# Kernel tuning notes

Hardware: AMD Instinct MI355X
Metric: run time of the kernel (lower is better)

Reference implementation:

```python
import jax, jax.numpy as jnp
import numpy as np

IN_DIM = 5
HIDDEN = 256
NUM_LAYERS = 2
OUT_DIM = 3
B, T = 256, 512


def setup_inputs() -> dict:
    key = jax.random.key(0)
    ks = jax.random.split(key, 16)
    s = 1.0 / np.sqrt(HIDDEN)  # PyTorch LSTM init scale
    inp = {
        "x": jax.random.normal(ks[0], (B, T, IN_DIM), dtype=jnp.float32),
        # layer 0 (input dim 5)
        "Wih0": jax.random.uniform(ks[1], (4 * HIDDEN, IN_DIM), minval=-s, maxval=s),
        "Whh0": jax.random.uniform(ks[2], (4 * HIDDEN, HIDDEN), minval=-s, maxval=s),
        "bih0": jax.random.uniform(ks[3], (4 * HIDDEN,), minval=-s, maxval=s),
        "bhh0": jax.random.uniform(ks[4], (4 * HIDDEN,), minval=-s, maxval=s),
        # layer 1 (input dim HIDDEN)
        "Wih1": jax.random.uniform(ks[5], (4 * HIDDEN, HIDDEN), minval=-s, maxval=s),
        "Whh1": jax.random.uniform(ks[6], (4 * HIDDEN, HIDDEN), minval=-s, maxval=s),
        "bih1": jax.random.uniform(ks[7], (4 * HIDDEN,), minval=-s, maxval=s),
        "bhh1": jax.random.uniform(ks[8], (4 * HIDDEN,), minval=-s, maxval=s),
        # head: Linear(HIDDEN, 3)
        "Wh": jax.random.uniform(ks[9], (OUT_DIM, HIDDEN), minval=-s, maxval=s),
        "bh": jax.random.uniform(ks[10], (OUT_DIM,), minval=-s, maxval=s),
    }
    return inp


def _lstm_layer(x, Wih, Whh, bih, bhh):
    # x: [B, T, D_in] -> h_seq: [B, T, H]
    Bn, Tn, _ = x.shape
    H = Whh.shape[1]
    # precompute input contribution for all timesteps: [T, B, 4H]
    pre = jnp.einsum("btd,gd->tbg", x, Wih) + bih + bhh

    def step(carry, gates_in):
        h, c = carry
        gates = gates_in + h @ Whh.T  # [B, 4H]
        i, f, g, o = jnp.split(gates, 4, axis=-1)  # PyTorch gate order
        i = jax.nn.sigmoid(i)
        f = jax.nn.sigmoid(f)
        g = jnp.tanh(g)
        o = jax.nn.sigmoid(o)
        c = f * c + i * g
        h = o * jnp.tanh(c)
        return (h, c), h

    h0 = jnp.zeros((Bn, H), dtype=x.dtype)
    c0 = jnp.zeros((Bn, H), dtype=x.dtype)
    _, h_seq = jax.lax.scan(step, (h0, c0), pre)  # h_seq: [T, B, H]
    return jnp.transpose(h_seq, (1, 0, 2))  # [B, T, H]


def reference(x, Wih0, Whh0, bih0, bhh0, Wih1, Whh1, bih1, bhh1, Wh, bh):
    h = _lstm_layer(x, Wih0, Whh0, bih0, bhh0)
    h = _lstm_layer(h, Wih1, Whh1, bih1, bhh1)
    # head applied pointwise; only the last timestep is kept, so apply to last step
    last = h[:, -1, :]  # [B, H]
    y = jax.nn.sigmoid(jax.nn.relu(last) @ Wh.T + bh)  # [B, 3]
    return y[:, None, :]  # [B, 1, 3]
```

## Files before the change

### kernel.cpp

```cpp
#include <hip/hip_runtime.h>
#include <hip/hip_bf16.h>

typedef unsigned short u16;
typedef signed char i8;
typedef __attribute__((ext_vector_type(4))) float f32x4;
typedef __attribute__((ext_vector_type(4))) int i32x4;
typedef __attribute__((ext_vector_type(8))) short bf16x8;
typedef __attribute__((ext_vector_type(2))) unsigned int u32x2;

#define HID 256
#define NG 1024
#define TSTEPS 512
#define BATCH 256
#define CH 32
#define NCH 16
#define BB 4
#define HSTR 288
#define LOG2E 1.4426950408889634f
#define PRE_TSTR 262144
#define H0C_TSTR 65536

#define GB0 128
#define GB1 160
#define NBLK 224

#define MFMA_BF16(a, b, c) __builtin_amdgcn_mfma_f32_16x16x32_bf16((a), (b), (c), 0, 0, 0)
#define MFMA_I8(a, b, c)   __builtin_amdgcn_mfma_i32_16x16x64_i8((a), (b), (c), 0, 0, 0)

__device__ __forceinline__ float rcpf_(float x) {
#if __has_builtin(__builtin_amdgcn_rcpf)
    return __builtin_amdgcn_rcpf(x);
#else
    return 1.f / x;
#endif
}
__device__ __forceinline__ float exp2_(float x) {
#if __has_builtin(__builtin_amdgcn_exp2f)
    return __builtin_amdgcn_exp2f(x);
#else
    return exp2f(x);
#endif
}
__device__ __forceinline__ float sigm2(float y) { return rcpf_(1.f + exp2_(-y)); }
__device__ __forceinline__ float tanh2(float y2) { return fmaf(-2.f, rcpf_(exp2_(y2) + 1.f), 1.f); }
__device__ __forceinline__ u16 f2bf(float v){ __hip_bfloat16 h=__float2bfloat16(v); return __builtin_bit_cast(u16,h); }
__device__ __forceinline__ float bf2f(u16 u){ unsigned x=((unsigned)u)<<16; return __builtin_bit_cast(float,x); }

__global__ void prep_a(const float* __restrict__ Whh0, const float* __restrict__ Whh1,
                       const float* __restrict__ bih0, const float* __restrict__ bhh0,
                       const float* __restrict__ bih1, const float* __restrict__ bhh1,
                       float* __restrict__ qs0, float* __restrict__ dq0s,
                       float* __restrict__ qs1, float* __restrict__ dq1s,
                       float* __restrict__ b0s, float* __restrict__ b1s) {
    int r = blockIdx.x * blockDim.x + threadIdx.x;
    if (r >= NG) return;
    float m0 = 1e-20f, m1 = 1e-20f;
    for (int k = 0; k < HID; k++) {
        m0 = fmaxf(m0, fabsf(Whh0[r * HID + k]));
        m1 = fmaxf(m1, fabsf(Whh1[r * HID + k]));
    }
    qs0[r] = 127.f / m0;   dq0s[r] = m0 / 16129.f * LOG2E;
    qs1[r] = 127.f / m1;   dq1s[r] = m1 / 16129.f * LOG2E;
    b0s[r] = (bih0[r] + bhh0[r]) * LOG2E;
    b1s[r] = (bih1[r] + bhh1[r]) * LOG2E;
}

__global__ void prep_b(const float* __restrict__ x,
    const float* __restrict__ Wih0, const float* __restrict__ Whh0,
    const float* __restrict__ Wih1, const float* __restrict__ Whh1,
    const float* __restrict__ qs0, const float* __restrict__ qs1,
    i8* __restrict__ wi80, i8* __restrict__ wi81,
    u16* __restrict__ wih1f, u16* __restrict__ wih0f,
    i8* __restrict__ hs0, i8* __restrict__ hs1,
    float* __restrict__ cs0, float* __restrict__ cs1, u16* __restrict__ xpad)
{
    const int stride = gridDim.x * blockDim.x;
    const int tid = blockIdx.x * blockDim.x + threadIdx.x;
    for (int i = tid; i < NG * HID; i += stride) {
        int e = i & 15, l = (i >> 4) & 63, kc = (i >> 10) & 3, gt = i >> 12;
        int row = 16 * gt + (l & 15);
        int k = kc * 64 + (l >> 4) * 16 + e;
        float q0 = __builtin_rintf(Whh0[row * HID + k] * qs0[row]);
        float q1 = __builtin_rintf(Whh1[row * HID + k] * qs1[row]);
        wi80[i] = (i8)fminf(fmaxf(q0, -127.f), 127.f);
        wi81[i] = (i8)fminf(fmaxf(q1, -127.f), 127.f);
    }
    for (int i = tid; i < NG * HID; i += stride) {
        int gt = i >> 12, kk = (i >> 9) & 7, l = (i >> 3) & 63, e = i & 7;
        wih1f[i] = f2bf(Wih1[(16 * gt + (l & 15)) * HID + kk * 32 + (l >> 4) * 8 + e] * LOG2E);
    }
    for (int i = tid; i < 32768; i += stride) {
        int gt = i >> 9, l = (i >> 3) & 63, e = i & 7;
        int k = (l >> 4) * 8 + e;
        wih0f[i] = (k < 5) ? f2bf(Wih0[(16 * gt + (l & 15)) * 5 + k] * LOG2E) : (u16)0;
    }
    for (int i = tid; i < TSTEPS * BATCH * 8; i += stride) {
        int tok = i >> 3, k = i & 7, t = tok >> 8, b = tok & 255;
        xpad[i] = (k < 5) ? f2bf(x[((size_t)b * TSTEPS + t) * 5 + k]) : (u16)0;
    }
    for (int i = tid; i < BATCH * HID; i += stride) { hs0[i] = 0; hs1[i] = 0; cs0[i] = 0.f; cs1[i] = 0.f; }
}

__global__ __launch_bounds__(1024) __attribute__((amdgpu_waves_per_eu(4, 4)))
void stage_fused(int L,
    const u16* __restrict__ xpad8, const u16* __restrict__ wih0f, const float* __restrict__ b0s,
    const u16* __restrict__ wih1f, const float* __restrict__ b1s,
    u16* __restrict__ p0w, const u16* __restrict__ p0r,
    u16* __restrict__ h0w, const u16* __restrict__ h0r,
    u16* __restrict__ p1w, const u16* __restrict__ p1r,
    const i8* __restrict__ wi80, const i8* __restrict__ wi81,
    const float* __restrict__ dq0s, const float* __restrict__ dq1s,
    i8* __restrict__ hs0, i8* __restrict__ hs1,
    float* __restrict__ cs0, float* __restrict__ cs1)
{
    __shared__ __align__(16) char smem[16384];
    const int bid = blockIdx.x;
    const int tid = threadIdx.x, lane = tid & 63;
    const int col = lane & 15, kgrp = lane >> 4;

    if (bid < GB0) {
        const int layer = bid >> 6;
        if (layer == 0) { if (L < 1 || L > NCH) return; }
        else            { if (L < 3 || L > NCH + 2) return; }
        i8 (*h_lds)[BB * HSTR] = (i8 (*)[BB * HSTR])smem;
        const int btile = bid & 63;
        const u16* pre   = layer ? p1r : p0r;
        const i8*  wi8   = layer ? wi81 : wi80;
        const float* dq  = layer ? dq1s : dq0s;
        i8*    h_state   = layer ? hs1 : hs0;
        float* c_state   = layer ? cs1 : cs0;
        const int w = tid >> 6;
        const int b0 = btile * BB;
        const int u = w * 16 + col;

        float sc[4];
        i32x4 wv[4][4];
#pragma unroll
        for (int j = 0; j < 4; j++) {
            const int gt = 16 * j + w;
            sc[j] = dq[gt * 16 + col];
#pragma unroll
            for (int kc = 0; kc < 4; kc++)
                wv[j][kc] = ((const i32x4*)wi8)[(gt * 4 + kc) * 64 + lane];
        }
        if (tid < 64 * BB) {
            const int rrow = tid >> 6, cc = (tid & 63) * 4;
            *(int*)&h_lds[0][rrow * HSTR + cc] = *(const int*)&h_state[(b0 + rrow) * HID + cc];
        }
        float c_reg = c_state[(size_t)(b0 + kgrp) * HID + u];

        const u16* pb = pre + ((size_t)btile << 12) + (u << 2) + kgrp;
        u16 pvA[4], pvB[4];
#pragma unroll
        for (int j = 0; j < 4; j++) pvA[j] = pb[j << 10];
        const size_t h0base = ((((size_t)(w >> 1) * 16 + (btile >> 2)) * 4
                               + ((w & 1) * 2 + (col >> 3))) * 16
                              + ((btile & 3) * 4 + kgrp)) * 8 + (col & 7);
        __syncthreads();

#define REC_STEP(T, CUR, PVC, PVN) do {                                             \
        _Pragma("unroll")                                                           \
        for (int j = 0; j < 4; j++)                                                 \
            asm volatile("" : "+v"(wv[j][0]), "+v"(wv[j][1]),                       \
                              "+v"(wv[j][2]), "+v"(wv[j][3]));                      \
        i32x4 acc[4];                                                               \
        _Pragma("unroll")                                                           \
        for (int j = 0; j < 4; j++) acc[j] = (i32x4){0, 0, 0, 0};                   \
        _Pragma("unroll")                                                           \
        for (int kc = 0; kc < 4; kc++) {                                            \
            i32x4 a_ = *(const i32x4*)&h_lds[CUR][(col >> 2) * HSTR + kc * 64 + kgrp * 16]; \
            _Pragma("unroll")                                                       \
            for (int j = 0; j < 4; j++) acc[j] = MFMA_I8(a_, wv[j][kc], acc[j]);    \
        }                                                                           \
        const int tn_ = ((T) + 1 < CH) ? (T) + 1 : (T);                             \
        _Pragma("unroll")                                                           \
        for (int j = 0; j < 4; j++) PVN[j] = pb[(size_t)tn_ * PRE_TSTR + (j << 10)];\
        const float yi = fmaf((float)acc[0][0], sc[0], bf2f(PVC[0]));               \
        const float yf = fmaf((float)acc[1][0], sc[1], bf2f(PVC[1]));               \
        const float yg = fmaf((float)acc[2][0], sc[2], bf2f(PVC[2]));               \
        const float yo = fmaf((float)acc[3][0], sc[3], bf2f(PVC[3]));               \
        const float iv = sigm2(yi), fv = sigm2(yf), ov = sigm2(yo);                 \
        const float gv = tanh2(yg + yg);                                            \
        const float cn = fmaf(fv, c_reg, iv * gv);                                  \
        c_reg = cn;                                                                 \
        const float hv = ov * tanh2(cn * (2.f * LOG2E));                            \
        h_lds[(CUR) ^ 1][kgrp * HSTR + u] = (i8)__float2int_rn(hv * 127.f);         \
        if (layer == 0)                                                             \
            h0w[h0base + (size_t)(T) * H0C_TSTR] = f2bf(hv);                        \
        asm volatile("s_waitcnt lgkmcnt(0)" ::: "memory");                          \
        __builtin_amdgcn_s_barrier();                                               \
        __builtin_amdgcn_sched_barrier(0);                                          \
    } while (0)

#pragma unroll 1
        for (int t2 = 0; t2 < CH; t2 += 2) {
            REC_STEP(t2,     0, pvA, pvB);
            REC_STEP(t2 + 1, 1, pvB, pvA);
        }
#undef REC_STEP

        c_state[(size_t)(b0 + kgrp) * HID + u] = c_reg;
        if (tid < 64 * BB) {
            const int rrow = tid >> 6, cc = (tid & 63) * 4;
            *(int*)&h_state[(b0 + rrow) * HID + cc] = *(const int*)&h_lds[0][rrow * HSTR + cc];
        }
        return;
    } else if (bid < GB1) {
        if (L >= NCH) return;
        const int tp = bid - GB0;
        const int w = tid >> 6;
        const int j = w >> 2;
        float bias[4];
        bf16x8 wv4[4];
#pragma unroll
        for (int tm = 0; tm < 4; tm++) {
            const int tile = w * 4 + tm;
            bias[tm] = b0s[tile * 16 + col];
            wv4[tm] = *(const bf16x8*)&wih0f[((size_t)tile * 64 + lane) * 8];
        }
        const u16* Ab = xpad8 + ((size_t)L * CH + tp) * BATCH * 8;
#pragma unroll 1
        for (int btg = 0; btg < 16; btg++) {
            bf16x8 af = {0, 0, 0, 0, 0, 0, 0, 0};
            if (kgrp == 0) af = *(const bf16x8*)&Ab[(btg * 16 + col) * 8];
            f32x4 acc[4];
#pragma unroll
            for (int tm = 0; tm < 4; tm++) acc[tm] = (f32x4){bias[tm], bias[tm], bias[tm], bias[tm]};
#pragma unroll
            for (int tm = 0; tm < 4; tm++) acc[tm] = MFMA_BF16(af, wv4[tm], acc[tm]);
#pragma unroll
            for (int tm = 0; tm < 4; tm++) {
                const int ul = ((w & 3) * 4 + tm) * 16 + col;
                const size_t off = ((((size_t)tp * 64 + btg * 4 + kgrp) * 4 + j) << 10) + (ul << 2);
                u32x2 pk;
                pk.x = (unsigned)f2bf(acc[tm][0]) | ((unsigned)f2bf(acc[tm][1]) << 16);
                pk.y = (unsigned)f2bf(acc[tm][2]) | ((unsigned)f2bf(acc[tm][3]) << 16);
                *(u32x2*)&p0w[off] = pk;
            }
        }
        return;
    } else {
        if (L < 2 || L > NCH + 1) return;
        const int g = bid - GB1;
        const int j = g & 3;
        const int tpb = (g >> 2) * 2;
        const int w = tid >> 6;
        const int gt = j * 16 + w;
        const float bias = b1s[gt * 16 + col];
        bf16x8 wv8[8];
#pragma unroll
        for (int kk = 0; kk < 8; kk++)
            wv8[kk] = *(const bf16x8*)&wih1f[((size_t)(gt * 8 + kk) * 64 + lane) * 8];
        u16* As = (u16*)smem;
        const int kks = tid >> 7;
        const int e4 = (tid & 127) * 4;
#pragma unroll 1
        for (int tpi = 0; tpi < 2; tpi++) {
            const int tp = tpb + tpi;
            const u16* Asrc = h0r + (size_t)tp * H0C_TSTR;
            {
                u32x2 st = *(const u32x2*)&Asrc[((size_t)kks * 16 + 0) * 512 + e4];
                *(u32x2*)&As[kks * 512 + e4] = st;
            }
            __syncthreads();
#pragma unroll 1
            for (int bt = 0; bt < 16; bt++) {
                const int cur = bt & 1, nxt = cur ^ 1;
                u32x2 nx;
                if (bt + 1 < 16)
                    nx = *(const u32x2*)&Asrc[((size_t)kks * 16 + bt + 1) * 512 + e4];
                bf16x8 a8[8];
#pragma unroll
                for (int kk = 0; kk < 8; kk++)
                    a8[kk] = *(const bf16x8*)&As[cur * 4096 + kk * 512 + lane * 8];
                f32x4 acc = (f32x4){bias, bias, bias, bias};
#pragma unroll
                for (int kk = 0; kk < 8; kk++)
                    acc = MFMA_BF16(a8[kk], wv8[kk], acc);
                const int ul = w * 16 + col;
                const size_t off = ((((size_t)tp * 64 + bt * 4 + kgrp) * 4 + j) << 10) + (ul << 2);
                u32x2 pk;
                pk.x = (unsigned)f2bf(acc[0]) | ((unsigned)f2bf(acc[1]) << 16);
                pk.y = (unsigned)f2bf(acc[2]) | ((unsigned)f2bf(acc[3]) << 16);
                *(u32x2*)&p1w[off] = pk;
                if (bt + 1 < 16)
                    *(u32x2*)&As[nxt * 4096 + kks * 512 + e4] = nx;
                __syncthreads();
            }
        }
        return;
    }
}

__global__ void head_kernel(const i8* __restrict__ hs1,
                            const float* __restrict__ Wh, const float* __restrict__ bh,
                            float* __restrict__ y) {
    int b = blockIdx.x;
    int l = threadIdx.x;
    const float inv127 = 1.f / 127.f;
    float hr[4];
#pragma unroll
    for (int i = 0; i < 4; ++i) hr[i] = fmaxf((float)hs1[b * HID + l + 64 * i] * inv127, 0.f);
    for (int o = 0; o < 3; ++o) {
        float s = 0.f;
#pragma unroll
        for (int i = 0; i < 4; ++i) s += hr[i] * Wh[o * HID + l + 64 * i];
        for (int off = 32; off > 0; off >>= 1) s += __shfl_down(s, off, 64);
        if (l == 0) y[b * 3 + o] = 1.f / (1.f + exp2_(-(s + bh[o]) * LOG2E));
    }
}

extern "C" void kernel_launch(void* const* d_in, const int* in_sizes, int n_in,
                              void* d_out, int out_size, void* d_ws, size_t ws_size,
                              hipStream_t stream) {
    const float* x    = (const float*)d_in[0];
    const float* Wih0 = (const float*)d_in[1];
    const float* Whh0 = (const float*)d_in[2];
    const float* bih0 = (const float*)d_in[3];
    const float* bhh0 = (const float*)d_in[4];
    const float* Wih1 = (const float*)d_in[5];
    const float* Whh1 = (const float*)d_in[6];
    const float* bih1 = (const float*)d_in[7];
    const float* bhh1 = (const float*)d_in[8];
    const float* Wh   = (const float*)d_in[9];
    const float* bh   = (const float*)d_in[10];

    char* ws = (char*)d_ws;
    i8*    wi80  = (i8*)(ws);
    i8*    wi81  = (i8*)(ws + ((size_t)256 << 10));
    u16*   wih1f = (u16*)(ws + ((size_t)512 << 10));
    u16*   wih0f = (u16*)(ws + ((size_t)1024 << 10));
    float* qs0   = (float*)(ws + ((size_t)1088 << 10));
    float* dq0s  = (float*)(ws + ((size_t)1092 << 10));
    float* qs1   = (float*)(ws + ((size_t)1096 << 10));
    float* dq1s  = (float*)(ws + ((size_t)1100 << 10));
    float* b0s   = (float*)(ws + ((size_t)1104 << 10));
    float* b1s   = (float*)(ws + ((size_t)1108 << 10));
    i8*    hs0   = (i8*)(ws + ((size_t)1112 << 10));
    i8*    hs1   = (i8*)(ws + ((size_t)1176 << 10));
    float* cs0   = (float*)(ws + ((size_t)1240 << 10));
    float* cs1   = (float*)(ws + ((size_t)1496 << 10));
    u16*   xpad  = (u16*)(ws + ((size_t)1752 << 10));
    u16*   h0c   = (u16*)(ws + ((size_t)4096 << 10));
    u16*   pre0  = (u16*)(ws + ((size_t)12288 << 10));
    u16*   pre1  = (u16*)(ws + ((size_t)45056 << 10));
    const size_t PRE_ELE = (size_t)CH * BATCH * NG;
    const size_t H0C_ELE = (size_t)CH * BATCH * HID;

    prep_a<<<4, 256, 0, stream>>>(Whh0, Whh1, bih0, bhh0, bih1, bhh1,
                                  qs0, dq0s, qs1, dq1s, b0s, b1s);
    prep_b<<<1024, 256, 0, stream>>>(x, Wih0, Whh0, Wih1, Whh1, qs0, qs1,
                                     wi80, wi81, wih1f, wih0f, hs0, hs1, cs0, cs1, xpad);
    for (int L = 0; L <= NCH + 2; L++) {
        const size_t pA = (size_t)(L & 1), pB = pA ^ 1;
        stage_fused<<<NBLK, 1024, 0, stream>>>(L, xpad, wih0f, b0s, wih1f, b1s,
            pre0 + pA * PRE_ELE,
            pre0 + pB * PRE_ELE,
            h0c  + pB * H0C_ELE,
            h0c  + pA * H0C_ELE,
            pre1 + pA * PRE_ELE,
            pre1 + pB * PRE_ELE,
            wi80, wi81, dq0s, dq1s, hs0, hs1, cs0, cs1);
    }
    head_kernel<<<BATCH, 64, 0, stream>>>(hs1, Wh, bh, (float*)d_out);
}
```

Baseline: 566.0 us.

## Fuse layer-0 input projection into recurrent step, drop pre0 buffer and a pipeline stage

Layer 0's input projection (dimension 5) is now computed inline in each recurrent timestep with scalar FMAs from xpad, instead of running in separate MFMA blocks that wrote a bf16 pre0 buffer. This drops the 32 x-projection blocks, the pre0 global traffic and one stage from the launch pipeline (NCH+2 launches instead of NCH+3), shortening the serial launch chain. In exchange, the layer-0 recurrent critical path gains about 20 FMAs and a global x load per step, and pre1 and h0c buffer indexing is reshuffled.

After: 773.7 us. 1.37x slower.

```diff
diff --git a/kernel.cpp b/kernel.cpp
--- a/kernel.cpp
+++ b/kernel.cpp
@@ -20,9 +20,8 @@
 #define PRE_TSTR 262144
 #define H0C_TSTR 65536
 
-#define GB0 128
-#define GB1 160
-#define NBLK 224
+#define GB1 128
+#define NBLK 192
 
 #define MFMA_BF16(a, b, c) __builtin_amdgcn_mfma_f32_16x16x32_bf16((a), (b), (c), 0, 0, 0)
 #define MFMA_I8(a, b, c)   __builtin_amdgcn_mfma_i32_16x16x64_i8((a), (b), (c), 0, 0, 0)
@@ -70,7 +69,7 @@
     const float* __restrict__ Wih1, const float* __restrict__ Whh1,
     const float* __restrict__ qs0, const float* __restrict__ qs1,
     i8* __restrict__ wi80, i8* __restrict__ wi81,
-    u16* __restrict__ wih1f, u16* __restrict__ wih0f,
+    u16* __restrict__ wih1f, u16* __restrict__ w0c,
     i8* __restrict__ hs0, i8* __restrict__ hs1,
     float* __restrict__ cs0, float* __restrict__ cs1, u16* __restrict__ xpad)
 {
@@ -89,10 +88,9 @@
         int gt = i >> 12, kk = (i >> 9) & 7, l = (i >> 3) & 63, e = i & 7;
         wih1f[i] = f2bf(Wih1[(16 * gt + (l & 15)) * HID + kk * 32 + (l >> 4) * 8 + e] * LOG2E);
     }
-    for (int i = tid; i < 32768; i += stride) {
-        int gt = i >> 9, l = (i >> 3) & 63, e = i & 7;
-        int k = (l >> 4) * 8 + e;
-        wih0f[i] = (k < 5) ? f2bf(Wih0[(16 * gt + (l & 15)) * 5 + k] * LOG2E) : (u16)0;
+    for (int i = tid; i < NG * 8; i += stride) {
+        int r = i >> 3, k = i & 7;
+        w0c[i] = (k < 5) ? f2bf(Wih0[r * 5 + k] * LOG2E) : (u16)0;
     }
     for (int i = tid; i < TSTEPS * BATCH * 8; i += stride) {
         int tok = i >> 3, k = i & 7, t = tok >> 8, b = tok & 255;
@@ -103,9 +101,8 @@
 
 __global__ __launch_bounds__(1024) __attribute__((amdgpu_waves_per_eu(4, 4)))
 void stage_fused(int L,
-    const u16* __restrict__ xpad8, const u16* __restrict__ wih0f, const float* __restrict__ b0s,
+    const u16* __restrict__ xpad8, const u16* __restrict__ w0c, const float* __restrict__ b0s,
     const u16* __restrict__ wih1f, const float* __restrict__ b1s,
-    u16* __restrict__ p0w, const u16* __restrict__ p0r,
     u16* __restrict__ h0w, const u16* __restrict__ h0r,
     u16* __restrict__ p1w, const u16* __restrict__ p1r,
     const i8* __restrict__ wi80, const i8* __restrict__ wi81,
@@ -118,47 +115,120 @@
     const int tid = threadIdx.x, lane = tid & 63;
     const int col = lane & 15, kgrp = lane >> 4;
 
-    if (bid < GB0) {
+    if (bid < GB1) {
         const int layer = bid >> 6;
-        if (layer == 0) { if (L < 1 || L > NCH) return; }
-        else            { if (L < 3 || L > NCH + 2) return; }
+        const int btile = bid & 63;
         i8 (*h_lds)[BB * HSTR] = (i8 (*)[BB * HSTR])smem;
-        const int btile = bid & 63;
-        const u16* pre   = layer ? p1r : p0r;
-        const i8*  wi8   = layer ? wi81 : wi80;
-        const float* dq  = layer ? dq1s : dq0s;
-        i8*    h_state   = layer ? hs1 : hs0;
-        float* c_state   = layer ? cs1 : cs0;
         const int w = tid >> 6;
         const int b0 = btile * BB;
         const int u = w * 16 + col;
 
-        float sc[4];
-        i32x4 wv[4][4];
-#pragma unroll
-        for (int j = 0; j < 4; j++) {
-            const int gt = 16 * j + w;
-            sc[j] = dq[gt * 16 + col];
-#pragma unroll
-            for (int kc = 0; kc < 4; kc++)
-                wv[j][kc] = ((const i32x4*)wi8)[(gt * 4 + kc) * 64 + lane];
-        }
-        if (tid < 64 * BB) {
-            const int rrow = tid >> 6, cc = (tid & 63) * 4;
-            *(int*)&h_lds[0][rrow * HSTR + cc] = *(const int*)&h_state[(b0 + rrow) * HID + cc];
-        }
-        float c_reg = c_state[(size_t)(b0 + kgrp) * HID + u];
-
-        const u16* pb = pre + ((size_t)btile << 12) + (u << 2) + kgrp;
-        u16 pvA[4], pvB[4];
-#pragma unroll
-        for (int j = 0; j < 4; j++) pvA[j] = pb[j << 10];
-        const size_t h0base = ((((size_t)(w >> 1) * 16 + (btile >> 2)) * 4
-                               + ((w & 1) * 2 + (col >> 3))) * 16
-                              + ((btile & 3) * 4 + kgrp)) * 8 + (col & 7);
-        __syncthreads();
-
-#define REC_STEP(T, CUR, PVC, PVN) do {                                             \
+        if (layer == 0) {
+            if (L >= NCH) return;
+            float sc[4], pbias[4], w0r[4][5];
+            i32x4 wv[4][4];
+#pragma unroll
+            for (int j = 0; j < 4; j++) {
+                const int gt = 16 * j + w;
+                sc[j] = dq0s[gt * 16 + col];
+                pbias[j] = b0s[gt * 16 + col];
+                bf16x8 wrow = *(const bf16x8*)&w0c[(j * 256 + u) * 8];
+#pragma unroll
+                for (int k = 0; k < 5; k++) w0r[j][k] = bf2f((u16)wrow[k]);
+#pragma unroll
+                for (int kc = 0; kc < 4; kc++)
+                    wv[j][kc] = ((const i32x4*)wi80)[(gt * 4 + kc) * 64 + lane];
+            }
+            if (tid < 64 * BB) {
+                const int rrow = tid >> 6, cc = (tid & 63) * 4;
+                *(int*)&h_lds[0][rrow * HSTR + cc] = *(const int*)&hs0[(b0 + rrow) * HID + cc];
+            }
+            float c_reg = cs0[(size_t)(b0 + kgrp) * HID + u];
+            const u16* xb = xpad8 + (((size_t)L * CH) * 256 + (b0 + kgrp)) * 8;
+            bf16x8 xvA, xvB;
+            xvA = *(const bf16x8*)&xb[0];
+            const size_t h0base = ((((size_t)(w >> 1) * 16 + (btile >> 2)) * 4
+                                   + ((w & 1) * 2 + (col >> 3))) * 16
+                                  + ((btile & 3) * 4 + kgrp)) * 8 + (col & 7);
+            __syncthreads();
+
+#define REC_STEP0(T, CUR, XC, XN) do {                                              \
+        _Pragma("unroll")                                                           \
+        for (int j = 0; j < 4; j++)                                                 \
+            asm volatile("" : "+v"(wv[j][0]), "+v"(wv[j][1]),                       \
+                              "+v"(wv[j][2]), "+v"(wv[j][3]));                      \
+        i32x4 acc[4];                                                               \
+        _Pragma("unroll")                                                           \
+        for (int j = 0; j < 4; j++) acc[j] = (i32x4){0, 0, 0, 0};                   \
+        _Pragma("unroll")                                                           \
+        for (int kc = 0; kc < 4; kc++) {                                            \
+            i32x4 a_ = *(const i32x4*)&h_lds[CUR][(col >> 2) * HSTR + kc * 64 + kgrp * 16]; \
+            _Pragma("unroll")                                                       \
+            for (int j = 0; j < 4; j++) acc[j] = MFMA_I8(a_, wv[j][kc], acc[j]);    \
+        }                                                                           \
+        const int tn_ = ((T) + 1 < CH) ? (T) + 1 : (T);                             \
+        XN = *(const bf16x8*)&xb[(size_t)tn_ * 2048];                               \
+        float xf[5], p[4];                                                          \
+        _Pragma("unroll")                                                           \
+        for (int k = 0; k < 5; k++) xf[k] = bf2f((u16)XC[k]);                       \
+        _Pragma("unroll")                                                           \
+        for (int j = 0; j < 4; j++) {                                               \
+            p[j] = pbias[j];                                                        \
+            _Pragma("unroll")                                                       \
+            for (int k = 0; k < 5; k++) p[j] = fmaf(w0r[j][k], xf[k], p[j]);        \
+        }                                                                           \
+        const float yi = fmaf((float)acc[0][0], sc[0], p[0]);                       \
+        const float yf = fmaf((float)acc[1][0], sc[1], p[1]);                       \
+        const float yg = fmaf((float)acc[2][0], sc[2], p[2]);                       \
+        const float yo = fmaf((float)acc[3][0], sc[3], p[3]);                       \
+        const float iv = sigm2(yi), fv = sigm2(yf), ov = sigm2(yo);                 \
+        const float gv = tanh2(yg + yg);                                            \
+        const float cn = fmaf(fv, c_reg, iv * gv);                                  \
+        c_reg = cn;                                                                 \
+        const float hv = ov * tanh2(cn * (2.f * LOG2E));                            \
+        h_lds[(CUR) ^ 1][kgrp * HSTR + u] = (i8)__float2int_rn(hv * 127.f);         \
+        h0w[h0base + (size_t)(T) * H0C_TSTR] = f2bf(hv);                            \
+        asm volatile("s_waitcnt lgkmcnt(0)" ::: "memory");                          \
+        __builtin_amdgcn_s_barrier();                                               \
+        __builtin_amdgcn_sched_barrier(0);                                          \
+    } while (0)
+
+#pragma unroll 1
+            for (int t2 = 0; t2 < CH; t2 += 2) {
+                REC_STEP0(t2,     0, xvA, xvB);
+                REC_STEP0(t2 + 1, 1, xvB, xvA);
+            }
+#undef REC_STEP0
+
+            cs0[(size_t)(b0 + kgrp) * HID + u] = c_reg;
+            if (tid < 64 * BB) {
+                const int rrow = tid >> 6, cc = (tid & 63) * 4;
+                *(int*)&hs0[(b0 + rrow) * HID + cc] = *(const int*)&h_lds[0][rrow * HSTR + cc];
+            }
+        } else {
+            if (L < 2 || L > NCH + 1) return;
+            float sc[4];
+            i32x4 wv[4][4];
+#pragma unroll
+            for (int j = 0; j < 4; j++) {
+                const int gt = 16 * j + w;
+                sc[j] = dq1s[gt * 16 + col];
+#pragma unroll
+                for (int kc = 0; kc < 4; kc++)
+                    wv[j][kc] = ((const i32x4*)wi81)[(gt * 4 + kc) * 64 + lane];
+            }
+            if (tid < 64 * BB) {
+                const int rrow = tid >> 6, cc = (tid & 63) * 4;
+                *(int*)&h_lds[0][rrow * HSTR + cc] = *(const int*)&hs1[(b0 + rrow) * HID + cc];
+            }
+            float c_reg = cs1[(size_t)(b0 + kgrp) * HID + u];
+            const u16* pb = p1r + ((size_t)btile << 12) + (u << 2) + kgrp;
+            u16 pvA[4], pvB[4];
+#pragma unroll
+            for (int j = 0; j < 4; j++) pvA[j] = pb[j << 10];
+            __syncthreads();
+
+#define REC_STEP1(T, CUR, PVC, PVN) do {                                            \
         _Pragma("unroll")                                                           \
         for (int j = 0; j < 4; j++)                                                 \
             asm volatile("" : "+v"(wv[j][0]), "+v"(wv[j][1]),                       \
@@ -185,62 +255,27 @@
         c_reg = cn;                                                                 \
         const float hv = ov * tanh2(cn * (2.f * LOG2E));                            \
         h_lds[(CUR) ^ 1][kgrp * HSTR + u] = (i8)__float2int_rn(hv * 127.f);         \
-        if (layer == 0)                                                             \
-            h0w[h0base + (size_t)(T) * H0C_TSTR] = f2bf(hv);                        \
         asm volatile("s_waitcnt lgkmcnt(0)" ::: "memory");                          \
         __builtin_amdgcn_s_barrier();                                               \
         __builtin_amdgcn_sched_barrier(0);                                          \
     } while (0)
 
 #pragma unroll 1
-        for (int t2 = 0; t2 < CH; t2 += 2) {
-            REC_STEP(t2,     0, pvA, pvB);
-            REC_STEP(t2 + 1, 1, pvB, pvA);
-        }
-#undef REC_STEP
-
-        c_state[(size_t)(b0 + kgrp) * HID + u] = c_reg;
-        if (tid < 64 * BB) {
-            const int rrow = tid >> 6, cc = (tid & 63) * 4;
-            *(int*)&h_state[(b0 + rrow) * HID + cc] = *(const int*)&h_lds[0][rrow * HSTR + cc];
-        }
-        return;
-    } else if (bid < GB1) {
-        if (L >= NCH) return;
-        const int tp = bid - GB0;
-        const int w = tid >> 6;
-        const int j = w >> 2;
-        float bias[4];
-        bf16x8 wv4[4];
-#pragma unroll
-        for (int tm = 0; tm < 4; tm++) {
-            const int tile = w * 4 + tm;
-            bias[tm] = b0s[tile * 16 + col];
-            wv4[tm] = *(const bf16x8*)&wih0f[((size_t)tile * 64 + lane) * 8];
-        }
-        const u16* Ab = xpad8 + ((size_t)L * CH + tp) * BATCH * 8;
-#pragma unroll 1
-        for (int btg = 0; btg < 16; btg++) {
-            bf16x8 af = {0, 0, 0, 0, 0, 0, 0, 0};
-            if (kgrp == 0) af = *(const bf16x8*)&Ab[(btg * 16 + col) * 8];
-            f32x4 acc[4];
-#pragma unroll
-            for (int tm = 0; tm < 4; tm++) acc[tm] = (f32x4){bias[tm], bias[tm], bias[tm], bias[tm]};
-#pragma unroll
-            for (int tm = 0; tm < 4; tm++) acc[tm] = MFMA_BF16(af, wv4[tm], acc[tm]);
-#pragma unroll
-            for (int tm = 0; tm < 4; tm++) {
-                const int ul = ((w & 3) * 4 + tm) * 16 + col;
-                const size_t off = ((((size_t)tp * 64 + btg * 4 + kgrp) * 4 + j) << 10) + (ul << 2);
-                u32x2 pk;
-                pk.x = (unsigned)f2bf(acc[tm][0]) | ((unsigned)f2bf(acc[tm][1]) << 16);
-                pk.y = (unsigned)f2bf(acc[tm][2]) | ((unsigned)f2bf(acc[tm][3]) << 16);
-                *(u32x2*)&p0w[off] = pk;
+            for (int t2 = 0; t2 < CH; t2 += 2) {
+                REC_STEP1(t2,     0, pvA, pvB);
+                REC_STEP1(t2 + 1, 1, pvB, pvA);
+            }
+#undef REC_STEP1
+
+            cs1[(size_t)(b0 + kgrp) * HID + u] = c_reg;
+            if (tid < 64 * BB) {
+                const int rrow = tid >> 6, cc = (tid & 63) * 4;
+                *(int*)&hs1[(b0 + rrow) * HID + cc] = *(const int*)&h_lds[0][rrow * HSTR + cc];
             }
         }
         return;
     } else {
-        if (L < 2 || L > NCH + 1) return;
+        if (L < 1 || L > NCH) return;
         const int g = bid - GB1;
         const int j = g & 3;
         const int tpb = (g >> 2) * 2;
@@ -329,7 +364,7 @@
     i8*    wi80  = (i8*)(ws);
     i8*    wi81  = (i8*)(ws + ((size_t)256 << 10));
     u16*   wih1f = (u16*)(ws + ((size_t)512 << 10));
-    u16*   wih0f = (u16*)(ws + ((size_t)1024 << 10));
+    u16*   w0c   = (u16*)(ws + ((size_t)1024 << 10));
     float* qs0   = (float*)(ws + ((size_t)1088 << 10));
     float* dq0s  = (float*)(ws + ((size_t)1092 << 10));
     float* qs1   = (float*)(ws + ((size_t)1096 << 10));
@@ -342,24 +377,20 @@
     float* cs1   = (float*)(ws + ((size_t)1496 << 10));
     u16*   xpad  = (u16*)(ws + ((size_t)1752 << 10));
     u16*   h0c   = (u16*)(ws + ((size_t)4096 << 10));
-    u16*   pre0  = (u16*)(ws + ((size_t)12288 << 10));
-    u16*   pre1  = (u16*)(ws + ((size_t)45056 << 10));
+    u16*   pre1  = (u16*)(ws + ((size_t)12288 << 10));
     const size_t PRE_ELE = (size_t)CH * BATCH * NG;
     const size_t H0C_ELE = (size_t)CH * BATCH * HID;
 
     prep_a<<<4, 256, 0, stream>>>(Whh0, Whh1, bih0, bhh0, bih1, bhh1,
                                   qs0, dq0s, qs1, dq1s, b0s, b1s);
     prep_b<<<1024, 256, 0, stream>>>(x, Wih0, Whh0, Wih1, Whh1, qs0, qs1,
-                                     wi80, wi81, wih1f, wih0f, hs0, hs1, cs0, cs1, xpad);
-    for (int L = 0; L <= NCH + 2; L++) {
-        const size_t pA = (size_t)(L & 1), pB = pA ^ 1;
-        stage_fused<<<NBLK, 1024, 0, stream>>>(L, xpad, wih0f, b0s, wih1f, b1s,
-            pre0 + pA * PRE_ELE,
-            pre0 + pB * PRE_ELE,
-            h0c  + pB * H0C_ELE,
-            h0c  + pA * H0C_ELE,
-            pre1 + pA * PRE_ELE,
-            pre1 + pB * PRE_ELE,
+                                     wi80, wi81, wih1f, w0c, hs0, hs1, cs0, cs1, xpad);
+    for (int L = 0; L <= NCH + 1; L++) {
+        stage_fused<<<NBLK, 1024, 0, stream>>>(L, xpad, w0c, b0s, wih1f, b1s,
+            h0c  + (size_t)(L & 1) * H0C_ELE,
+            h0c  + (size_t)((L + 1) & 1) * H0C_ELE,
+            pre1 + (size_t)((L + 1) & 1) * PRE_ELE,
+            pre1 + (size_t)(L & 1) * PRE_ELE,
             wi80, wi81, dq0s, dq1s, hs0, hs1, cs0, cs1);
     }
     head_kernel<<<BATCH, 64, 0, stream>>>(hs1, Wh, bh, (float*)d_out);
```
